# Performance work log

Hardware: AMD Instinct MI355X
Metric: run time of the kernel (lower is better)

Reference implementation:

```python
import jax, jax.numpy as jnp
import numpy as np

NH = 8  # num_heads


def _conv1x1(w, b, x):
    # 1x1 conv == channel matmul: w [O,C], x [B,C,H,W]
    return jnp.einsum('oc,bchw->bohw', w, x) + b[None, :, None, None]


def _fwd(low_freq_feat, high_freq_feat, ext_context, road_feat,
         ext_proj_w, ext_proj_b, road_proj_w, road_proj_b,
         ext_qkv_w, ext_qkv_b, road_qkv_w, road_qkv_b,
         ext_out_w, ext_out_b, road_out_w, road_out_b,
         gate_ext_w, gate_ext_b, gate_road_w, gate_road_b):
    B, C, H, W = low_freq_feat.shape
    nh = NH
    hd = C // nh
    HW = H * W
    scale = hd ** -0.5

    ext_p = ext_context @ ext_proj_w.T + ext_proj_b          # [B,C]
    road_p = _conv1x1(road_proj_w, road_proj_b, road_feat)   # [B,C,H,W]

    eqkv = (ext_p @ ext_qkv_w.T + ext_qkv_b).reshape(B, 3, nh, hd)
    ext_q, ext_v = eqkv[:, 0], eqkv[:, 2]                    # [B,nh,hd]

    # torch: conv out [B,3C,H,W] viewed as (B,C,3,H,W) -> q/k/v interleaved over channels
    rqkv = _conv1x1(road_qkv_w, road_qkv_b, road_p).reshape(B, C, 3, H, W)
    road_k = rqkv[:, :, 1].reshape(B, nh, hd, HW).transpose(0, 1, 3, 2)  # [B,nh,HW,hd]
    road_v = rqkv[:, :, 2].reshape(B, nh, hd, HW).transpose(0, 1, 3, 2)

    # ext->road attention. The torch code expands ext_q to HW identical rows; one row
    # per (batch, head) gives a bit-identical result without the [B,nh,HW,HW] blowup.
    scores = jnp.einsum('bnd,bnpd->bnp', ext_q, road_k) * scale
    attn = jax.nn.softmax(scores, axis=-1)                   # [B,nh,HW]
    ext_head = jnp.einsum('bnp,bnpd->bnd', attn, road_v).reshape(B, C)
    ext_vec = ext_head @ ext_out_w.T + ext_out_b             # [B,C]
    ext_feat_spatial = jnp.broadcast_to(ext_vec[:, :, None, None], (B, C, H, W))

    # road->ext attention: all HW keys/values are copies of the single ext token, so
    # softmax is exactly uniform and the output per position is exactly ext_v. The
    # road_out 1x1 conv on a spatially-constant map is a single matvec per batch.
    road_vec = ext_v.reshape(B, C) @ road_out_w.T + road_out_b
    road_enhanced = jnp.broadcast_to(road_vec[:, :, None, None], (B, C, H, W))

    # gated fusion (ext stream): spatial mean of constant map == ext_vec
    gate_in = jnp.concatenate([low_freq_feat.mean(axis=(2, 3)), ext_vec], axis=-1)
    ext_gate = jax.nn.sigmoid(gate_in @ gate_ext_w.T + gate_ext_b)[:, :, None, None]
    ext_final = low_freq_feat * (1.0 - ext_gate) + ext_feat_spatial * ext_gate

    # gated fusion (road stream)
    rg_in = jnp.concatenate([high_freq_feat, road_enhanced], axis=1)  # [B,2C,H,W]
    road_gate = jax.nn.sigmoid(_conv1x1(gate_road_w, gate_road_b, rg_in))
    road_final = high_freq_feat * (1.0 - road_gate) + road_enhanced * road_gate
    return ext_final, road_final


def setup_inputs() -> dict:
    key = jax.random.key(0)
    ks = jax.random.split(key, 20)
    B, C, H, W, E = 8, 256, 64, 64, 64
    f = lambda k, shape, s=1.0: jax.random.normal(k, shape, dtype=jnp.float32) * s
    return {
        'low_freq_feat': f(ks[0], (B, C, H, W)),
        'high_freq_feat': f(ks[1], (B, C, H, W)),
        'ext_context': f(ks[2], (B, E)),
        'road_feat': f(ks[3], (B, C, H, W)),
        'ext_proj_w': f(ks[4], (C, E), 0.05), 'ext_proj_b': f(ks[5], (C,), 0.02),
        'road_proj_w': f(ks[6], (C, C), 0.05), 'road_proj_b': f(ks[7], (C,), 0.02),
        'ext_qkv_w': f(ks[8], (3 * C, C), 0.05), 'ext_qkv_b': f(ks[9], (3 * C,), 0.02),
        'road_qkv_w': f(ks[10], (3 * C, C), 0.05), 'road_qkv_b': f(ks[11], (3 * C,), 0.02),
        'ext_out_w': f(ks[12], (C, C), 0.05), 'ext_out_b': f(ks[13], (C,), 0.02),
        'road_out_w': f(ks[14], (C, C), 0.05), 'road_out_b': f(ks[15], (C,), 0.02),
        'gate_ext_w': f(ks[16], (C, 2 * C), 0.05), 'gate_ext_b': f(ks[17], (C,), 0.02),
        'gate_road_w': f(ks[18], (C, 2 * C), 0.05), 'gate_road_b': f(ks[19], (C,), 0.02),
    }


def reference(low_freq_feat, high_freq_feat, ext_context, road_feat,
              ext_proj_w, ext_proj_b, road_proj_w, road_proj_b,
              ext_qkv_w, ext_qkv_b, road_qkv_w, road_qkv_b,
              ext_out_w, ext_out_b, road_out_w, road_out_b,
              gate_ext_w, gate_ext_b, gate_road_w, gate_road_b):
    return _fwd(low_freq_feat, high_freq_feat, ext_context, road_feat,
                ext_proj_w, ext_proj_b, road_proj_w, road_proj_b,
                ext_qkv_w, ext_qkv_b, road_qkv_w, road_qkv_b,
                ext_out_w, ext_out_b, road_out_w, road_out_b,
                gate_ext_w, gate_ext_b, gate_road_w, gate_road_b)
```

## Files before the change

### kernel.cpp

```cpp
#include <hip/hip_runtime.h>

typedef short bf16x8 __attribute__((ext_vector_type(8)));
typedef float f32x4 __attribute__((ext_vector_type(4)));

__device__ __forceinline__ unsigned short f2b(float f) {
    unsigned int u = __builtin_bit_cast(unsigned int, f);
    unsigned int r = u + 0x7FFFu + ((u >> 16) & 1u);
    return (unsigned short)(r >> 16);
}
__device__ __forceinline__ float wsum64(float v) {
    #pragma unroll
    for (int m = 32; m; m >>= 1) v += __shfl_xor(v, m, 64);
    return v;
}


__global__ __launch_bounds__(256) void k_setup(const float* __restrict__ w1,
                                               const float* __restrict__ wqkv,
                                               const float* __restrict__ b1,
                                               const float* __restrict__ bqkv,
                                               const float* __restrict__ gate_road_w,
                                               const float* __restrict__ ext_proj_w,
                                               const float* __restrict__ ext_qkv_w,
                                               const float* __restrict__ road_out_w,
                                               const float* __restrict__ ext_out_w,
                                               const float* __restrict__ gate_ext_w,
                                               const float* __restrict__ low,
                                               unsigned short* __restrict__ W3b,
                                               unsigned short* __restrict__ Wcb,
                                               unsigned short* __restrict__ WF,
                                               float* __restrict__ bcv,
                                               float* __restrict__ mean_low) {
    int bid = blockIdx.x, t = threadIdx.x;
    __shared__ float sel[8][256];
    __shared__ float red[8][4];
    if (bid >= 448) {
        int bc = bid - 448;
        const f32x4* p4 = (const f32x4*)(low + (size_t)bc * 4096);
        float s = 0.f;
        for (int i = t; i < 1024; i += 256) {
            f32x4 v = p4[i];
            s += v[0] + v[1] + v[2] + v[3];
        }
        s = wsum64(s);
        if ((t & 63) == 0) red[0][t >> 6] = s;
        __syncthreads();
        if (t == 0) mean_low[bc] = (red[0][0] + red[0][1] + red[0][2] + red[0][3]) * (1.0f / 4096.0f);
    } else if (bid < 256) {
        int i = bid * 256 + t;
        int o = i >> 8, k = i & 255;
        W3b[i] = f2b(gate_road_w[o * 512 + k]);
    } else if (bid < 320) {
        int o0 = (bid - 256) * 8;
        #pragma unroll
        for (int r = 0; r < 8; r++) {
            int o = o0 + r;
            int c = (o < 256) ? o : o - 256;
            int g = (o < 256) ? 1 : 2;
            sel[r][t] = wqkv[(size_t)(3 * c + g) * 256 + t];
        }
        __syncthreads();
        float b1v = b1[t];
        #pragma unroll
        for (int r = 0; r < 8; r++) {
            float v = wsum64(sel[r][t] * b1v);
            if ((t & 63) == 0) red[r][t >> 6] = v;
        }
        __syncthreads();
        if (t < 8) {
            int o = o0 + t;
            int c = (o < 256) ? o : o - 256;
            int g = (o < 256) ? 1 : 2;
            bcv[o] = red[t][0] + red[t][1] + red[t][2] + red[t][3] + bqkv[3 * c + g];
        }
        float acc[8] = {};
        #pragma unroll 16
        for (int m = 0; m < 256; m++) {
            float w1v = w1[(size_t)m * 256 + t];
            #pragma unroll
            for (int r = 0; r < 8; r++) acc[r] += sel[r][m] * w1v;
        }
        #pragma unroll
        for (int r = 0; r < 8; r++) Wcb[(size_t)(o0 + r) * 256 + t] = f2b(acc[r]);
    } else {
        int mb = bid - 320;
        int m = mb >> 4, ctile = mb & 15;
        const float* src;
        int stride, K, coff;
        unsigned short* dst;
        switch (m) {
        case 0: src = ext_qkv_w;                     stride = 256; K = 256; coff = 0;   dst = WF;          break;
        case 1: src = ext_qkv_w + (size_t)512 * 256; stride = 256; K = 256; coff = 0;   dst = WF + 65536;  break;
        case 2: src = road_out_w;                    stride = 256; K = 256; coff = 0;   dst = WF + 131072; break;
        case 3: src = gate_road_w;                   stride = 512; K = 256; coff = 256; dst = WF + 196608; break;
        case 4: src = ext_proj_w;                    stride = 64;  K = 64;  coff = 0;   dst = WF + 262144; break;
        case 5: src = ext_out_w;                     stride = 256; K = 256; coff = 0;   dst = WF + 278528; break;
        case 6: src = gate_ext_w;                    stride = 512; K = 256; coff = 0;   dst = WF + 344064; break;
        default: src = gate_ext_w;                   stride = 512; K = 256; coff = 256; dst = WF + 409600; break;
        }
        int lc = t >> 4, kseg = t & 15;
        int k0 = kseg * 16;
        if (k0 < K) {
            int c = ctile * 16 + lc;
            const float* sp = src + (size_t)c * stride + coff + k0;
            f32x4 v0 = *(const f32x4*)sp;
            f32x4 v1 = *(const f32x4*)(sp + 4);
            f32x4 v2 = *(const f32x4*)(sp + 8);
            f32x4 v3 = *(const f32x4*)(sp + 12);
            int kk = kseg >> 1;
            int Kt = K >> 5;
            #pragma unroll
            for (int h = 0; h < 2; h++) {
                int lhi = (kseg & 1) * 2 + h;
                int lane = lhi * 16 + lc;
                bf16x8 o;
                f32x4 a = h ? v2 : v0, b = h ? v3 : v1;
                #pragma unroll
                for (int i = 0; i < 4; i++) { o[i] = (short)f2b(a[i]); o[4 + i] = (short)f2b(b[i]); }
                *(bf16x8*)(dst + ((size_t)(ctile * Kt + kk) << 9) + lane * 8) = o;
            }
        }
    }
}

__global__ __launch_bounds__(256) void k_tiny(const unsigned short* __restrict__ WF,
                                              const float* __restrict__ ext_context,
                                              const float* __restrict__ ext_proj_b,
                                              const float* __restrict__ ext_qkv_b,
                                              const float* __restrict__ road_out_b,
                                              const float* __restrict__ gate_road_b,
                                              float* __restrict__ ext_q,
                                              float* __restrict__ road_vec,
                                              float* __restrict__ rg_const) {
    __shared__ unsigned short xA[16][264];
    __shared__ unsigned short xB[16][264];
    int t = threadIdx.x;
    int w = t >> 6, lane = t & 63, l15 = lane & 15, lhi = lane >> 4;
    const unsigned short* WqF  = WF;
    const unsigned short* WvF  = WF + 65536;
    const unsigned short* WroF = WF + 131072;
    const unsigned short* WgF  = WF + 196608;
    const unsigned short* WpF  = WF + 262144;
    {
        int b = t >> 5, k0 = (t & 31) * 2;
        float c0v = ext_context[b * 64 + k0];
        float c1v = ext_context[b * 64 + k0 + 1];
        *(unsigned int*)&xA[b][k0] = (unsigned int)f2b(c0v) | ((unsigned int)f2b(c1v) << 16);
    }
    __syncthreads();
    {
        f32x4 acc[4] = {};
        #pragma unroll
        for (int kk = 0; kk < 2; kk++) {
            bf16x8 a = *(const bf16x8*)&xA[l15][kk * 32 + 8 * lhi];
            #pragma unroll
            for (int ni = 0; ni < 4; ni++) {
                int ct = w * 4 + ni;
                bf16x8 bfr = *(const bf16x8*)(WpF + ((size_t)(ct * 2 + kk) << 9) + lane * 8);
                acc[ni] = __builtin_amdgcn_mfma_f32_16x16x32_bf16(a, bfr, acc[ni], 0, 0, 0);
            }
        }
        if (lhi < 2) {
            #pragma unroll
            for (int ni = 0; ni < 4; ni++) {
                int c = w * 64 + ni * 16 + l15;
                float bp = ext_proj_b[c];
                #pragma unroll
                for (int r = 0; r < 4; r++)
                    xB[4 * lhi + r][c] = f2b(acc[ni][r] + bp);
            }
        }
    }
    __syncthreads();
    {
        f32x4 acc[8] = {};
        bool isq = (w < 2);
        int cbase = (w & 1) * 128;
        const unsigned short* Wb = isq ? WqF : WvF;
        for (int kk = 0; kk < 8; kk++) {
            bf16x8 a = *(const bf16x8*)&xB[l15][kk * 32 + 8 * lhi];
            #pragma unroll
            for (int ni = 0; ni < 8; ni++) {
                int ct = (cbase >> 4) + ni;
                bf16x8 bfr = *(const bf16x8*)(Wb + ((size_t)(ct * 8 + kk) << 9) + lane * 8);
                acc[ni] = __builtin_amdgcn_mfma_f32_16x16x32_bf16(a, bfr, acc[ni], 0, 0, 0);
            }
        }
        if (lhi < 2) {
            #pragma unroll
            for (int ni = 0; ni < 8; ni++) {
                int c = cbase + ni * 16 + l15;
                float bb = ext_qkv_b[(isq ? 0 : 512) + c];
                #pragma unroll
                for (int r = 0; r < 4; r++) {
                    int b = 4 * lhi + r;
                    float val = acc[ni][r] + bb;
                    if (isq) ext_q[b * 256 + c] = val;
                    else     xA[b][c] = f2b(val);
                }
            }
        }
    }
    __syncthreads();
    {
        f32x4 acc[4] = {};
        for (int kk = 0; kk < 8; kk++) {
            bf16x8 a = *(const bf16x8*)&xA[l15][kk * 32 + 8 * lhi];
            #pragma unroll
            for (int ni = 0; ni < 4; ni++) {
                int ct = w * 4 + ni;
                bf16x8 bfr = *(const bf16x8*)(WroF + ((size_t)(ct * 8 + kk) << 9) + lane * 8);
                acc[ni] = __builtin_amdgcn_mfma_f32_16x16x32_bf16(a, bfr, acc[ni], 0, 0, 0);
            }
        }
        if (lhi < 2) {
            #pragma unroll
            for (int ni = 0; ni < 4; ni++) {
                int c = w * 64 + ni * 16 + l15;
                float bb = road_out_b[c];
                #pragma unroll
                for (int r = 0; r < 4; r++) {
                    int b = 4 * lhi + r;
                    float val = acc[ni][r] + bb;
                    road_vec[b * 256 + c] = val;
                    xB[b][c] = f2b(val);
                }
            }
        }
    }
    __syncthreads();
    {
        f32x4 acc[4] = {};
        for (int kk = 0; kk < 8; kk++) {
            bf16x8 a = *(const bf16x8*)&xB[l15][kk * 32 + 8 * lhi];
            #pragma unroll
            for (int ni = 0; ni < 4; ni++) {
                int ct = w * 4 + ni;
                bf16x8 bfr = *(const bf16x8*)(WgF + ((size_t)(ct * 8 + kk) << 9) + lane * 8);
                acc[ni] = __builtin_amdgcn_mfma_f32_16x16x32_bf16(a, bfr, acc[ni], 0, 0, 0);
            }
        }
        if (lhi < 2) {
            #pragma unroll
            for (int ni = 0; ni < 4; ni++) {
                int c = w * 64 + ni * 16 + l15;
                float bb = gate_road_b[c];
                #pragma unroll
                for (int r = 0; r < 4; r++)
                    rg_const[(4 * lhi + r) * 256 + c] = acc[ni][r] + bb;
            }
        }
    }
}

__global__ __launch_bounds__(512) void k_kv(const float* __restrict__ road_feat,
                                            const unsigned short* __restrict__ Wcb,
                                            const float* __restrict__ bcv,
                                            const float* __restrict__ extq,
                                            float* __restrict__ part) {
    __shared__ unsigned short Xs[32 * 256];
    __shared__ float esh[8][32];
    char* Xc = (char*)Xs;
    int bid = blockIdx.x;
    int b  = bid >> 7;
    int p0 = (bid & 127) << 5;
    int t  = threadIdx.x;
    const float* rfb = road_feat + (size_t)b * 1048576;

    int c0 = 2 * (t >> 3);
    int j4 = (t & 7) * 4;
    #pragma unroll
    for (int it = 0; it < 2; ++it) {
        int c = c0 + 128 * it;
        f32x4 g0 = *(const f32x4*)(rfb + (size_t)c * 4096 + p0 + j4);
        f32x4 g1 = *(const f32x4*)(rfb + (size_t)(c + 1) * 4096 + p0 + j4);
        #pragma unroll
        for (int i = 0; i < 4; i++) {
            int j = j4 + i;
            unsigned int pk = (unsigned int)f2b(g0[i]) | ((unsigned int)f2b(g1[i]) << 16);
            *(unsigned int*)(Xc + ((j * 512 + 2 * c) ^ ((j & 15) << 4))) = pk;
        }
    }
    __syncthreads();

    int w = t >> 6, lane = t & 63, l15 = lane & 15, lhi = lane >> 4;

    f32x4 acc[2][4] = {};
    for (int kk = 0; kk < 8; kk++) {
        bf16x8 a[2];
        #pragma unroll
        for (int mi = 0; mi < 2; mi++) {
            int j = mi * 16 + l15;
            int off = (j * 512 + (kk * 32 + 8 * lhi) * 2) ^ ((j & 15) << 4);
            a[mi] = *(const bf16x8*)((const char*)Xs + off);
        }
        #pragma unroll
        for (int ni = 0; ni < 4; ni++) {
            int n = (ni < 2) ? (w * 32 + ni * 16 + l15) : (256 + w * 32 + (ni - 2) * 16 + l15);
            bf16x8 bf = *(const bf16x8*)(Wcb + (size_t)n * 256 + kk * 32 + 8 * lhi);
            acc[0][ni] = __builtin_amdgcn_mfma_f32_16x16x32_bf16(a[0], bf, acc[0][ni], 0, 0, 0);
            acc[1][ni] = __builtin_amdgcn_mfma_f32_16x16x32_bf16(a[1], bf, acc[1][ni], 0, 0, 0);
        }
    }

    float q0 = extq[b * 256 + w * 32 + l15];
    float q1 = extq[b * 256 + w * 32 + 16 + l15];
    float bk0 = bcv[w * 32 + l15];
    float bk1 = bcv[w * 32 + 16 + l15];
    #pragma unroll
    for (int mi = 0; mi < 2; mi++)
        #pragma unroll
        for (int r = 0; r < 4; r++) {
            int j = mi * 16 + 4 * lhi + r;
            float s = (acc[mi][0][r] + bk0) * q0 + (acc[mi][1][r] + bk1) * q1;
            s += __shfl_xor(s, 1, 64);
            s += __shfl_xor(s, 2, 64);
            s += __shfl_xor(s, 4, 64);
            s += __shfl_xor(s, 8, 64);
            if (l15 == 0)
                esh[w][j] = expf(s * 0.17677669529663687f);
        }

    float* pb = part + (size_t)bid * 264;
    {
        float v0 = esh[w][lane & 31];
        v0 += __shfl_xor(v0, 1, 64);
        v0 += __shfl_xor(v0, 2, 64);
        v0 += __shfl_xor(v0, 4, 64);
        v0 += __shfl_xor(v0, 8, 64);
        v0 += __shfl_xor(v0, 16, 64);
        if (lane == 0) pb[w] = v0;
    }
    #pragma unroll
    for (int vi = 0; vi < 2; vi++) {
        int cv = w * 32 + vi * 16 + l15;
        float bv = bcv[256 + cv];
        float p = 0.f;
        #pragma unroll
        for (int mi = 0; mi < 2; mi++)
            #pragma unroll
            for (int r = 0; r < 4; r++) {
                int j = mi * 16 + 4 * lhi + r;
                p += esh[w][j] * (acc[mi][2 + vi][r] + bv);
            }
        p += __shfl_xor(p, 16, 64);
        p += __shfl_xor(p, 32, 64);
        if (lhi == 0) pb[8 + cv] = p;
    }
}

__global__ __launch_bounds__(256) void k_vec_combine(const float* __restrict__ part,
                                                     float* __restrict__ hdg) {
    int b = blockIdx.x, c = threadIdx.x;
    __shared__ float tot[8];
    const float* pb = part + (size_t)b * 128 * 264;
    float a = 0.f;
    #pragma unroll 8
    for (int tile = 0; tile < 128; tile++) a += pb[tile * 264 + 8 + c];
    if (c < 8) {
        float s = 0.f;
        #pragma unroll 8
        for (int tile = 0; tile < 128; tile++) s += pb[tile * 264 + c];
        tot[c] = 1.0f / s;
    }
    __syncthreads();
    hdg[b * 256 + c] = a * tot[c >> 5];
}

__global__ __launch_bounds__(256) void k_vec2(const unsigned short* __restrict__ WF,
                                              const float* __restrict__ hdg,
                                              const float* __restrict__ mean_low,
                                              const float* __restrict__ ext_out_b,
                                              const float* __restrict__ gate_ext_b,
                                              float* __restrict__ ext_vec,
                                              float* __restrict__ ext_gate) {
    __shared__ unsigned short xA[16][264];
    __shared__ unsigned short xB[16][264];
    __shared__ unsigned short xC[16][264];
    int t = threadIdx.x;
    int w = t >> 6, lane = t & 63, l15 = lane & 15, lhi = lane >> 4;
    const unsigned short* WoF    = WF + 278528;
    const unsigned short* WgeLoF = WF + 344064;
    const unsigned short* WgeHiF = WF + 409600;
    {
        int bb = t >> 5, kb = t & 31;
        #pragma unroll
        for (int q = 0; q < 4; q++) {
            int k0 = (kb + 32 * q) * 2;
            *(unsigned int*)&xA[bb][k0] =
                (unsigned int)f2b(hdg[bb * 256 + k0]) | ((unsigned int)f2b(hdg[bb * 256 + k0 + 1]) << 16);
            *(unsigned int*)&xB[bb][k0] =
                (unsigned int)f2b(mean_low[bb * 256 + k0]) | ((unsigned int)f2b(mean_low[bb * 256 + k0 + 1]) << 16);
        }
    }
    __syncthreads();
    {
        f32x4 acc[4] = {};
        for (int kk = 0; kk < 8; kk++) {
            bf16x8 a = *(const bf16x8*)&xA[l15][kk * 32 + 8 * lhi];
            #pragma unroll
            for (int ni = 0; ni < 4; ni++) {
                int ct = w * 4 + ni;
                bf16x8 bfr = *(const bf16x8*)(WoF + ((size_t)(ct * 8 + kk) << 9) + lane * 8);
                acc[ni] = __builtin_amdgcn_mfma_f32_16x16x32_bf16(a, bfr, acc[ni], 0, 0, 0);
            }
        }
        if (lhi < 2) {
            #pragma unroll
            for (int ni = 0; ni < 4; ni++) {
                int c = w * 64 + ni * 16 + l15;
                float bb = ext_out_b[c];
                #pragma unroll
                for (int r = 0; r < 4; r++) {
                    int b = 4 * lhi + r;
                    float val = acc[ni][r] + bb;
                    ext_vec[b * 256 + c] = val;
                    xC[b][c] = f2b(val);
                }
            }
        }
    }
    __syncthreads();
    {
        f32x4 acc[4] = {};
        for (int kk = 0; kk < 8; kk++) {
            bf16x8 a = *(const bf16x8*)&xB[l15][kk * 32 + 8 * lhi];
            #pragma unroll
            for (int ni = 0; ni < 4; ni++) {
                int ct = w * 4 + ni;
                bf16x8 bfr = *(const bf16x8*)(WgeLoF + ((size_t)(ct * 8 + kk) << 9) + lane * 8);
                acc[ni] = __builtin_amdgcn_mfma_f32_16x16x32_bf16(a, bfr, acc[ni], 0, 0, 0);
            }
        }
        for (int kk = 0; kk < 8; kk++) {
            bf16x8 a = *(const bf16x8*)&xC[l15][kk * 32 + 8 * lhi];
            #pragma unroll
            for (int ni = 0; ni < 4; ni++) {
                int ct = w * 4 + ni;
                bf16x8 bfr = *(const bf16x8*)(WgeHiF + ((size_t)(ct * 8 + kk) << 9) + lane * 8);
                acc[ni] = __builtin_amdgcn_mfma_f32_16x16x32_bf16(a, bfr, acc[ni], 0, 0, 0);
            }
        }
        if (lhi < 2) {
            #pragma unroll
            for (int ni = 0; ni < 4; ni++) {
                int c = w * 64 + ni * 16 + l15;
                float bb = gate_ext_b[c];
                #pragma unroll
                for (int r = 0; r < 4; r++) {
                    int b = 4 * lhi + r;
                    ext_gate[b * 256 + c] = 1.0f / (1.0f + expf(-(acc[ni][r] + bb)));
                }
            }
        }
    }
}

__global__ __launch_bounds__(256) void k_ext_final(const float* __restrict__ low,
                                                   const float* __restrict__ ext_vec,
                                                   const float* __restrict__ ext_gate,
                                                   float* __restrict__ out) {
    int idx = blockIdx.x * 256 + threadIdx.x;
    #pragma unroll
    for (int rep = 0; rep < 4; ++rep) {
        int i = idx + rep * 524288;
        int bc = i >> 10;
        float g = ext_gate[bc];
        float vv = ext_vec[bc];
        f32x4 L = *(const f32x4*)(low + (size_t)i * 4);
        f32x4 o;
        #pragma unroll
        for (int c = 0; c < 4; c++) o[c] = L[c] + g * (vv - L[c]);
        *(f32x4*)(out + (size_t)i * 4) = o;
    }
}

__global__ __launch_bounds__(512) void k_road(const float* __restrict__ high,
                                              const unsigned short* __restrict__ W3b,
                                              const float* __restrict__ rg_const,
                                              const float* __restrict__ road_vec,
                                              float* __restrict__ outbuf) {
    __shared__ float Xs[32 * 256];
    char* Xc = (char*)Xs;
    int bid = blockIdx.x;
    int b  = bid >> 7;
    int p0 = (bid & 127) << 5;
    int t  = threadIdx.x;
    const float* hb = high + (size_t)b * 1048576;

    int c0 = t >> 3;
    int j4 = (t & 7) * 4;
    #pragma unroll
    for (int it = 0; it < 4; ++it) {
        int c = c0 + 64 * it;
        f32x4 g = *(const f32x4*)(hb + (size_t)c * 4096 + p0 + j4);
        #pragma unroll
        for (int i = 0; i < 4; i++) {
            int j = j4 + i;
            *(float*)(Xc + ((j * 1024 + 4 * c) ^ ((j & 15) << 4))) = g[i];
        }
    }
    __syncthreads();

    int w = t >> 6, lane = t & 63, l15 = lane & 15, lhi = lane >> 4;
    f32x4 acc[2][2] = {};
    for (int kk = 0; kk < 8; kk++) {
        bf16x8 a[2];
        #pragma unroll
        for (int mi = 0; mi < 2; mi++) {
            int j = mi * 16 + l15;
            int base = j * 1024 + (kk * 32 + 8 * lhi) * 4;
            int sw = (j & 15) << 4;
            f32x4 x0 = *(const f32x4*)(Xc + (base ^ sw));
            f32x4 x1 = *(const f32x4*)(Xc + ((base + 16) ^ sw));
            bf16x8 av;
            #pragma unroll
            for (int i = 0; i < 4; i++) {
                av[i]     = (short)f2b(x0[i]);
                av[4 + i] = (short)f2b(x1[i]);
            }
            a[mi] = av;
        }
        #pragma unroll
        for (int ni = 0; ni < 2; ni++) {
            int o = w * 32 + ni * 16 + l15;
            bf16x8 bf = *(const bf16x8*)(W3b + (size_t)o * 256 + kk * 32 + 8 * lhi);
            acc[0][ni] = __builtin_amdgcn_mfma_f32_16x16x32_bf16(a[0], bf, acc[0][ni], 0, 0, 0);
            acc[1][ni] = __builtin_amdgcn_mfma_f32_16x16x32_bf16(a[1], bf, acc[1][ni], 0, 0, 0);
        }
    }
    __syncthreads();

    #pragma unroll
    for (int ni = 0; ni < 2; ni++) {
        int o = w * 32 + ni * 16 + l15;
        float rc = rg_const[b * 256 + o];
        float rv = road_vec[b * 256 + o];
        #pragma unroll
        for (int mi = 0; mi < 2; mi++)
            #pragma unroll
            for (int r = 0; r < 4; r++) {
                int j = mi * 16 + 4 * lhi + r;
                float* slot = (float*)(Xc + ((j * 1024 + 4 * o) ^ ((j & 15) << 4)));
                float z = acc[mi][ni][r] + rc;
                float gte = 1.0f / (1.0f + expf(-z));
                float hv = *slot;
                *slot = hv + gte * (rv - hv);
            }
    }
    __syncthreads();

    float* ob = outbuf + 8388608 + (size_t)b * 1048576;
    #pragma unroll
    for (int it = 0; it < 4; ++it) {
        int c = c0 + 64 * it;
        f32x4 o4;
        #pragma unroll
        for (int i = 0; i < 4; i++) {
            int j = j4 + i;
            o4[i] = *(const float*)(Xc + ((j * 1024 + 4 * c) ^ ((j & 15) << 4)));
        }
        *(f32x4*)(ob + (size_t)c * 4096 + p0 + j4) = o4;
    }
}

extern "C" void kernel_launch(void* const* d_in, const int* in_sizes, int n_in,
                              void* d_out, int out_size, void* d_ws, size_t ws_size,
                              hipStream_t stream) {
    const float* low         = (const float*)d_in[0];
    const float* high        = (const float*)d_in[1];
    const float* ext_context = (const float*)d_in[2];
    const float* road_feat   = (const float*)d_in[3];
    const float* ext_proj_w  = (const float*)d_in[4];
    const float* ext_proj_b  = (const float*)d_in[5];
    const float* road_proj_w = (const float*)d_in[6];
    const float* road_proj_b = (const float*)d_in[7];
    const float* ext_qkv_w   = (const float*)d_in[8];
    const float* ext_qkv_b   = (const float*)d_in[9];
    const float* road_qkv_w  = (const float*)d_in[10];
    const float* road_qkv_b  = (const float*)d_in[11];
    const float* ext_out_w   = (const float*)d_in[12];
    const float* ext_out_b   = (const float*)d_in[13];
    const float* road_out_w  = (const float*)d_in[14];
    const float* road_out_b  = (const float*)d_in[15];
    const float* gate_ext_w  = (const float*)d_in[16];
    const float* gate_ext_b  = (const float*)d_in[17];
    const float* gate_road_w = (const float*)d_in[18];
    const float* gate_road_b = (const float*)d_in[19];

    float* out = (float*)d_out;
    unsigned short* wsb = (unsigned short*)d_ws;
    unsigned short* Wcb = wsb;
    unsigned short* W3b = wsb + 131072;
    float* fw = (float*)((char*)d_ws + 983040);
    float* ext_q    = fw;
    float* road_vec = fw + 2048;
    float* rg_const = fw + 4096;
    float* ext_vec  = fw + 8192;
    float* ext_gate = fw + 10240;
    float* mean_low = fw + 12288;
    float* bcv      = fw + 14336;
    float* hdg      = fw + 16384;
    float* part = out + 2097152;
    unsigned short* WF = (unsigned short*)(out + 4194304);

    k_setup<<<2496, 256, 0, stream>>>(road_proj_w, road_qkv_w, road_proj_b, road_qkv_b,
                                      gate_road_w, ext_proj_w, ext_qkv_w, road_out_w,
                                      ext_out_w, gate_ext_w, low,
                                      W3b, Wcb, WF, bcv, mean_low);
    k_tiny<<<1, 256, 0, stream>>>(WF, ext_context, ext_proj_b, ext_qkv_b,
                                  road_out_b, gate_road_b, ext_q, road_vec, rg_const);
    k_kv<<<1024, 512, 0, stream>>>(road_feat, Wcb, bcv, ext_q, part);
    k_vec_combine<<<8, 256, 0, stream>>>(part, hdg);
    k_vec2<<<1, 256, 0, stream>>>(WF, hdg, mean_low, ext_out_b, gate_ext_b,
                                  ext_vec, ext_gate);
    k_ext_final<<<2048, 256, 0, stream>>>(low, ext_vec, ext_gate, out);
    k_road<<<1024, 512, 0, stream>>>(high, W3b, rg_const, road_vec, out);
}
```

Before: 156.0 us.

## Fold ext query into key weights and defer value projection past reduction

```diff
diff --git a/kernel.cpp b/kernel.cpp
--- a/kernel.cpp
+++ b/kernel.cpp
@@ -2,11 +2,16 @@
 
 typedef short bf16x8 __attribute__((ext_vector_type(8)));
 typedef float f32x4 __attribute__((ext_vector_type(4)));
+
+#define ATT_SCALE 0.17677669529663687f
 
 __device__ __forceinline__ unsigned short f2b(float f) {
     unsigned int u = __builtin_bit_cast(unsigned int, f);
     unsigned int r = u + 0x7FFFu + ((u >> 16) & 1u);
     return (unsigned short)(r >> 16);
+}
+__device__ __forceinline__ float b2f(unsigned short v) {
+    return __builtin_bit_cast(float, (unsigned int)v << 16);
 }
 __device__ __forceinline__ float wsum64(float v) {
     #pragma unroll
@@ -253,13 +258,52 @@
     }
 }
 
-__global__ __launch_bounds__(512) void k_kv(const float* __restrict__ road_feat,
-                                            const unsigned short* __restrict__ Wcb,
-                                            const float* __restrict__ bcv,
-                                            const float* __restrict__ extq,
-                                            float* __restrict__ part) {
+__global__ __launch_bounds__(256) void k_qfold(const unsigned short* __restrict__ Wcb,
+                                               const float* __restrict__ bcv,
+                                               const float* __restrict__ ext_q,
+                                               unsigned short* __restrict__ wqf,
+                                               float* __restrict__ cqs) {
+    int b = blockIdx.x, t = threadIdx.x;
+    __shared__ float qs[256];
+    __shared__ float wq[8][256];
+    qs[t] = ext_q[b * 256 + t];
+    __syncthreads();
+    float acc[8] = {};
+    #pragma unroll
+    for (int h = 0; h < 8; h++)
+        #pragma unroll 8
+        for (int d = 0; d < 32; d++)
+            acc[h] += qs[h * 32 + d] * b2f(Wcb[(size_t)(h * 32 + d) * 256 + t]);
+    #pragma unroll
+    for (int h = 0; h < 8; h++) wq[h][t] = acc[h];
+    if (t < 8) {
+        float s = 0.f;
+        #pragma unroll 8
+        for (int d = 0; d < 32; d++) s += qs[t * 32 + d] * bcv[t * 32 + d];
+        cqs[b * 8 + t] = s * ATT_SCALE;
+    }
+    __syncthreads();
+    #pragma unroll
+    for (int q2 = 0; q2 < 2; q2++) {
+        int idx = t + 256 * q2;
+        int kk = idx >> 6, l = idx & 63;
+        int row = l & 15;
+        int kb = kk * 32 + (l >> 4) * 8;
+        bf16x8 o;
+        #pragma unroll
+        for (int e = 0; e < 8; e++)
+            o[e] = (row < 8) ? (short)f2b(wq[row][kb + e]) : (short)0;
+        *(bf16x8*)(wqf + ((size_t)(b * 8 + kk) * 64 + l) * 8) = o;
+    }
+}
+
+__global__ __launch_bounds__(256) void k_att(const float* __restrict__ road_feat,
+                                             const unsigned short* __restrict__ wqf,
+                                             const float* __restrict__ cqs,
+                                             float* __restrict__ part) {
     __shared__ unsigned short Xs[32 * 256];
-    __shared__ float esh[8][32];
+    __shared__ unsigned short Xt[256][40];
+    __shared__ float es_[8][36];
     char* Xc = (char*)Xs;
     int bid = blockIdx.x;
     int b  = bid >> 7;
@@ -270,101 +314,129 @@
     int c0 = 2 * (t >> 3);
     int j4 = (t & 7) * 4;
     #pragma unroll
-    for (int it = 0; it < 2; ++it) {
-        int c = c0 + 128 * it;
+    for (int it = 0; it < 4; ++it) {
+        int c = c0 + 64 * it;
         f32x4 g0 = *(const f32x4*)(rfb + (size_t)c * 4096 + p0 + j4);
         f32x4 g1 = *(const f32x4*)(rfb + (size_t)(c + 1) * 4096 + p0 + j4);
+        unsigned short h0[4], h1[4];
+        #pragma unroll
+        for (int i = 0; i < 4; i++) { h0[i] = f2b(g0[i]); h1[i] = f2b(g1[i]); }
         #pragma unroll
         for (int i = 0; i < 4; i++) {
             int j = j4 + i;
-            unsigned int pk = (unsigned int)f2b(g0[i]) | ((unsigned int)f2b(g1[i]) << 16);
+            unsigned int pk = (unsigned int)h0[i] | ((unsigned int)h1[i] << 16);
             *(unsigned int*)(Xc + ((j * 512 + 2 * c) ^ ((j & 15) << 4))) = pk;
         }
+        *(unsigned int*)&Xt[c][j4]         = (unsigned int)h0[0] | ((unsigned int)h0[1] << 16);
+        *(unsigned int*)&Xt[c][j4 + 2]     = (unsigned int)h0[2] | ((unsigned int)h0[3] << 16);
+        *(unsigned int*)&Xt[c + 1][j4]     = (unsigned int)h1[0] | ((unsigned int)h1[1] << 16);
+        *(unsigned int*)&Xt[c + 1][j4 + 2] = (unsigned int)h1[2] | ((unsigned int)h1[3] << 16);
     }
     __syncthreads();
 
     int w = t >> 6, lane = t & 63, l15 = lane & 15, lhi = lane >> 4;
 
-    f32x4 acc[2][4] = {};
-    for (int kk = 0; kk < 8; kk++) {
-        bf16x8 a[2];
-        #pragma unroll
-        for (int mi = 0; mi < 2; mi++) {
-            int j = mi * 16 + l15;
-            int off = (j * 512 + (kk * 32 + 8 * lhi) * 2) ^ ((j & 15) << 4);
-            a[mi] = *(const bf16x8*)((const char*)Xs + off);
-        }
-        #pragma unroll
-        for (int ni = 0; ni < 4; ni++) {
-            int n = (ni < 2) ? (w * 32 + ni * 16 + l15) : (256 + w * 32 + (ni - 2) * 16 + l15);
-            bf16x8 bf = *(const bf16x8*)(Wcb + (size_t)n * 256 + kk * 32 + 8 * lhi);
-            acc[0][ni] = __builtin_amdgcn_mfma_f32_16x16x32_bf16(a[0], bf, acc[0][ni], 0, 0, 0);
-            acc[1][ni] = __builtin_amdgcn_mfma_f32_16x16x32_bf16(a[1], bf, acc[1][ni], 0, 0, 0);
-        }
-    }
-
-    float q0 = extq[b * 256 + w * 32 + l15];
-    float q1 = extq[b * 256 + w * 32 + 16 + l15];
-    float bk0 = bcv[w * 32 + l15];
-    float bk1 = bcv[w * 32 + 16 + l15];
-    #pragma unroll
-    for (int mi = 0; mi < 2; mi++)
+    if (w < 2) {
+        f32x4 acc = {};
+        int px = w * 16 + l15;
+        for (int kk = 0; kk < 8; kk++) {
+            bf16x8 aq = *(const bf16x8*)(wqf + ((size_t)(b * 8 + kk) * 64 + lane) * 8);
+            bf16x8 bx = *(const bf16x8*)(Xc + ((px * 512 + (kk * 32 + 8 * lhi) * 2) ^ ((px & 15) << 4)));
+            acc = __builtin_amdgcn_mfma_f32_16x16x32_bf16(aq, bx, acc, 0, 0, 0);
+        }
         #pragma unroll
         for (int r = 0; r < 4; r++) {
-            int j = mi * 16 + 4 * lhi + r;
-            float s = (acc[mi][0][r] + bk0) * q0 + (acc[mi][1][r] + bk1) * q1;
-            s += __shfl_xor(s, 1, 64);
-            s += __shfl_xor(s, 2, 64);
-            s += __shfl_xor(s, 4, 64);
-            s += __shfl_xor(s, 8, 64);
-            if (l15 == 0)
-                esh[w][j] = expf(s * 0.17677669529663687f);
-        }
-
-    float* pb = part + (size_t)bid * 264;
-    {
-        float v0 = esh[w][lane & 31];
-        v0 += __shfl_xor(v0, 1, 64);
-        v0 += __shfl_xor(v0, 2, 64);
-        v0 += __shfl_xor(v0, 4, 64);
-        v0 += __shfl_xor(v0, 8, 64);
-        v0 += __shfl_xor(v0, 16, 64);
-        if (lane == 0) pb[w] = v0;
-    }
-    #pragma unroll
-    for (int vi = 0; vi < 2; vi++) {
-        int cv = w * 32 + vi * 16 + l15;
-        float bv = bcv[256 + cv];
-        float p = 0.f;
-        #pragma unroll
-        for (int mi = 0; mi < 2; mi++)
+            int row = 4 * lhi + r;
+            if (row < 8)
+                es_[row][w * 16 + l15] = expf(acc[r] * ATT_SCALE + cqs[b * 8 + row]);
+        }
+    }
+    __syncthreads();
+
+    float* pb = part + (size_t)bid * 2056;
+    {
+        float v = es_[t >> 5][t & 31];
+        v += __shfl_xor(v, 1, 64);
+        v += __shfl_xor(v, 2, 64);
+        v += __shfl_xor(v, 4, 64);
+        v += __shfl_xor(v, 8, 64);
+        v += __shfl_xor(v, 16, 64);
+        if ((lane & 31) == 0) pb[t >> 5] = v;
+    }
+    bf16x8 besv;
+    {
+        f32x4 e0 = *(const f32x4*)&es_[l15 & 7][8 * lhi];
+        f32x4 e1 = *(const f32x4*)&es_[l15 & 7][8 * lhi + 4];
+        #pragma unroll
+        for (int i = 0; i < 4; i++) { besv[i] = (short)f2b(e0[i]); besv[4 + i] = (short)f2b(e1[i]); }
+    }
+    #pragma unroll
+    for (int mf = 0; mf < 4; mf++) {
+        int f = w * 4 + mf;
+        int c = f * 16 + l15;
+        bf16x8 ax = *(const bf16x8*)&Xt[c][8 * lhi];
+        f32x4 acc = {};
+        acc = __builtin_amdgcn_mfma_f32_16x16x32_bf16(ax, besv, acc, 0, 0, 0);
+        if (l15 < 8) {
             #pragma unroll
             for (int r = 0; r < 4; r++) {
-                int j = mi * 16 + 4 * lhi + r;
-                p += esh[w][j] * (acc[mi][2 + vi][r] + bv);
-            }
-        p += __shfl_xor(p, 16, 64);
-        p += __shfl_xor(p, 32, 64);
-        if (lhi == 0) pb[8 + cv] = p;
-    }
-}
-
-__global__ __launch_bounds__(256) void k_vec_combine(const float* __restrict__ part,
-                                                     float* __restrict__ hdg) {
-    int b = blockIdx.x, c = threadIdx.x;
-    __shared__ float tot[8];
-    const float* pb = part + (size_t)b * 128 * 264;
-    float a = 0.f;
-    #pragma unroll 8
-    for (int tile = 0; tile < 128; tile++) a += pb[tile * 264 + 8 + c];
-    if (c < 8) {
-        float s = 0.f;
-        #pragma unroll 8
-        for (int tile = 0; tile < 128; tile++) s += pb[tile * 264 + c];
-        tot[c] = 1.0f / s;
-    }
-    __syncthreads();
-    hdg[b * 256 + c] = a * tot[c >> 5];
+                int cout = f * 16 + 4 * lhi + r;
+                pb[8 + cout * 8 + l15] = acc[r];
+            }
+        }
+    }
+}
+
+__global__ __launch_bounds__(256) void k_comb(const float* __restrict__ part,
+                                              const unsigned short* __restrict__ Wcb,
+                                              const float* __restrict__ bcv,
+                                              float* __restrict__ hdg) {
+    int b = blockIdx.x, t = threadIdx.x;
+    __shared__ float Yt[8][260];
+    __shared__ float S[8];
+    const float* pbase = part + (size_t)b * 128 * 2056;
+    float acc[9] = {};
+    for (int tile = 0; tile < 128; tile++) {
+        const float* pb = pbase + (size_t)tile * 2056;
+        #pragma unroll
+        for (int i = 0; i < 8; i++) acc[i] += pb[t + 256 * i];
+        if (t < 8) acc[8] += pb[2048 + t];
+    }
+    #pragma unroll
+    for (int i = 0; i < 8; i++) {
+        int idx = t + 256 * i;
+        if (idx >= 8) {
+            int c = (idx - 8) >> 3, h = (idx - 8) & 7;
+            Yt[h][c] = acc[i];
+        }
+    }
+    if (t < 8) S[t] = acc[8];
+    __syncthreads();
+    if (t < 8) S[t] = acc[0];
+    __syncthreads();
+    int w = t >> 6, lane = t & 63, l15 = lane & 15, lhi = lane >> 4;
+    float invS = 1.0f / S[l15 & 7];
+    #pragma unroll
+    for (int mf = 0; mf < 4; mf++) {
+        int f = w * 4 + mf;
+        f32x4 acc4 = {};
+        for (int kk = 0; kk < 8; kk++) {
+            bf16x8 aw = *(const bf16x8*)(Wcb + (size_t)(256 + f * 16 + l15) * 256 + kk * 32 + 8 * lhi);
+            f32x4 y0 = *(const f32x4*)&Yt[l15 & 7][kk * 32 + 8 * lhi];
+            f32x4 y1 = *(const f32x4*)&Yt[l15 & 7][kk * 32 + 8 * lhi + 4];
+            bf16x8 by;
+            #pragma unroll
+            for (int i = 0; i < 4; i++) { by[i] = (short)f2b(y0[i]); by[4 + i] = (short)f2b(y1[i]); }
+            acc4 = __builtin_amdgcn_mfma_f32_16x16x32_bf16(aw, by, acc4, 0, 0, 0);
+        }
+        if (l15 == (f >> 1)) {
+            #pragma unroll
+            for (int r = 0; r < 4; r++) {
+                int row = f * 16 + 4 * lhi + r;
+                hdg[b * 256 + row] = acc4[r] * invS + bcv[256 + row];
+            }
+        }
+    }
 }
 
 __global__ __launch_bounds__(256) void k_vec2(const unsigned short* __restrict__ WF,
@@ -601,8 +673,10 @@
     float* mean_low = fw + 12288;
     float* bcv      = fw + 14336;
     float* hdg      = fw + 16384;
+    float* cqs      = fw + 18432;
+    unsigned short* wqf = (unsigned short*)(fw + 18496);
     float* part = out + 2097152;
-    unsigned short* WF = (unsigned short*)(out + 4194304);
+    unsigned short* WF = (unsigned short*)(out + 4210688);
 
     k_setup<<<2496, 256, 0, stream>>>(road_proj_w, road_qkv_w, road_proj_b, road_qkv_b,
                                       gate_road_w, ext_proj_w, ext_qkv_w, road_out_w,
@@ -610,8 +684,9 @@
                                       W3b, Wcb, WF, bcv, mean_low);
     k_tiny<<<1, 256, 0, stream>>>(WF, ext_context, ext_proj_b, ext_qkv_b,
                                   road_out_b, gate_road_b, ext_q, road_vec, rg_const);
-    k_kv<<<1024, 512, 0, stream>>>(road_feat, Wcb, bcv, ext_q, part);
-    k_vec_combine<<<8, 256, 0, stream>>>(part, hdg);
+    k_qfold<<<8, 256, 0, stream>>>(Wcb, bcv, ext_q, wqf, cqs);
+    k_att<<<1024, 256, 0, stream>>>(road_feat, wqf, cqs, part);
+    k_comb<<<8, 256, 0, stream>>>(part, Wcb, bcv, hdg);
     k_vec2<<<1, 256, 0, stream>>>(WF, hdg, mean_low, ext_out_b, gate_ext_b,
                                   ext_vec, ext_gate);
     k_ext_final<<<2048, 256, 0, stream>>>(low, ext_vec, ext_gate, out);
```

Measured after the change: 202.4 us. +29.8%, slower.
